# Kernel optimization log

Hardware: AMD Instinct MI355X
Metric: run time of the kernel (lower is better)

The kernel has to match this reference:

```python
import jax, jax.numpy as jnp
import numpy as np
from jax import lax

# Config (matches init_kwargs)
B, CIN, H, W = 32, 256, 56, 56
COUT, KS, STRIDE, PAD, GROUPS = 256, 3, 1, 1, 2
CG_IN = CIN // GROUPS            # 128
OUT_F = COUT // GROUPS           # 128 per-group out features
IN_F = CG_IN * KS * KS           # 1152 per-group in features
Q = (IN_F * OUT_F // 4) * GROUPS # 73728 quadruplets total
TAU = 1.0

# All six 2-of-4 masking patterns (as in the torch module)
_MASK_PATTERNS = np.array([[0.,0.,1.,1.],[0.,1.,0.,1.],[0.,1.,1.,0.],
                           [1.,0.,0.,1.],[1.,0.,1.,0.],[1.,1.,0.,0.]], dtype=np.float32)


def setup_inputs() -> dict:
    key = jax.random.key(0)
    k1, k2, k3, k4 = jax.random.split(key, 4)
    x = jax.random.normal(k1, (B, CIN, H, W), dtype=jnp.float32)
    # per-group weight blocks, xavier-ish scale
    Ws = jax.random.normal(k2, (GROUPS, OUT_F, IN_F), dtype=jnp.float32) * 0.03
    choice_weights = jax.random.normal(k3, (Q, 6), dtype=jnp.float32)
    # gumbel noise: -log(Exp(1)) ~ Gumbel(0,1), matching -empty.exponential_().log()
    gumbels = -jnp.log(jax.random.exponential(k4, (Q, 6), dtype=jnp.float32))
    masking_patterns = jnp.asarray(_MASK_PATTERNS)
    return {"x": x, "Ws": Ws, "choice_weights": choice_weights,
            "gumbels": gumbels, "masking_patterns": masking_patterns}


def _hard_gumbel_softmax(logits, gumbels, tau):
    # straight-through hard gumbel softmax over last dim
    y_soft = jax.nn.softmax((logits + gumbels) / tau, axis=-1)
    idx = jnp.argmax(y_soft, axis=-1)
    y_hard = jax.nn.one_hot(idx, logits.shape[-1], dtype=logits.dtype)
    return y_hard - lax.stop_gradient(y_soft) + y_soft


def reference(x, Ws, choice_weights, gumbels, masking_patterns):
    # 1) sample 2:4 mask per quadruplet via hard gumbel-softmax choice over 6 patterns
    choice = _hard_gumbel_softmax(choice_weights, gumbels, TAU)   # (Q, 6)
    mask = choice @ masking_patterns                              # (Q, 4)
    mask = mask.reshape(GROUPS, OUT_F, IN_F)                      # quadruplets tile W row-major
    Wm = Ws * mask                                                # (G, OUT_F, IN_F)

    # 2) im2col (torch Unfold ordering: channel-major, then kh, kw)
    patches = lax.conv_general_dilated_patches(
        x, filter_shape=(KS, KS), window_strides=(STRIDE, STRIDE),
        padding=[(PAD, PAD), (PAD, PAD)])                         # (B, CIN*KS*KS, Ho, Wo)
    Ho = (H + 2 * PAD - KS) // STRIDE + 1
    Wo = (W + 2 * PAD - KS) // STRIDE + 1
    L = Ho * Wo
    # channel-major ordering => group g occupies contiguous IN_F rows
    patches = patches.reshape(B, GROUPS, IN_F, L)                 # (B, G, IN_F, L)

    # 3) per-group masked GEMM, no bias (use_bias=False)
    y = jnp.einsum('goi,bgil->bgol', Wm, patches)                 # (B, G, OUT_F, L)
    return y.reshape(B, COUT, Ho, Wo)
```

## Files before the change

kernel.cpp:

```cpp
#include <hip/hip_runtime.h>


#define INF   1152
#define HO    56
#define LOUT  3136
#define XP    58
#define Q     73728

typedef __attribute__((ext_vector_type(8))) short bf16x8;
typedef __attribute__((ext_vector_type(4))) float f32x4;

__device__ __forceinline__ unsigned short f2bf(float f) {
  union { float f; unsigned u; } v; v.f = f;
  unsigned r = v.u + 0x7fffu + ((v.u >> 16) & 1u);
  return (unsigned short)(r >> 16);
}

__device__ __forceinline__ void async_load16(const void* g, void* l) {
  __builtin_amdgcn_global_load_lds(
      (const __attribute__((address_space(1))) void*)g,
      (__attribute__((address_space(3))) void*)l, 16, 0, 0);
}

__global__ __launch_bounds__(256) void gumbel_kernel(
    const float* __restrict__ cw, const float* __restrict__ gb,
    unsigned char* __restrict__ pmask) {
  int q = blockIdx.x * 256 + threadIdx.x;
  const float* cq = cw + q * 6;
  const float* gq = gb + q * 6;
  float best = cq[0] + gq[0]; int bi = 0;
  #pragma unroll
  for (int j = 1; j < 6; ++j) {
    float v = cq[j] + gq[j];
    if (v > best) { best = v; bi = j; }
  }
  pmask[q] = (unsigned char)bi;
}

__global__ __launch_bounds__(256) void pack_kernel(
    const float* __restrict__ Ws, const unsigned char* __restrict__ pmask,
    const float* __restrict__ pat, unsigned short* __restrict__ Wt) {
  int idx = blockIdx.x * 256 + threadIdx.x;
  int c   = idx & 127;
  int of  = (idx >> 7) & 127;
  int gt  = idx >> 14;
  int g   = gt / 9;
  int tap = gt - g * 9;
  int e   = ((g << 7) + of) * INF + c * 9 + tap;
  float m = pat[pmask[e >> 2] * 4 + (e & 3)];
  Wt[idx] = f2bf(Ws[e] * m);
}

__global__ __launch_bounds__(256) void xpose_kernel(const float* __restrict__ x,
                                                    unsigned short* __restrict__ Xt) {
  __shared__ float lds[56 * 129];
  const int t   = threadIdx.x;
  const int ihp = blockIdx.x;
  const int bg  = blockIdx.y;
  uint4* dst = (uint4*)(Xt + ((bg * XP + ihp) * XP) * 128);
  if (ihp == 0 || ihp == XP - 1) {
    const uint4 z = {0u, 0u, 0u, 0u};
    for (int i = t; i < XP * 16; i += 256) dst[i] = z;
    return;
  }
  const int ih = ihp - 1;
  const float4* src = (const float4*)(x + (bg * 128) * LOUT + ih * HO);
  for (int i = t; i < 128 * 14; i += 256) {
    int c = i / 14, seg = i - c * 14;
    float4 v = src[c * (LOUT / 4) + seg];
    float* row = &lds[(seg * 4) * 129 + c];
    row[0]       = v.x;
    row[129]     = v.y;
    row[2 * 129] = v.z;
    row[3 * 129] = v.w;
  }
  __syncthreads();
  for (int i = t; i < XP * 16; i += 256) {
    int iwp = i >> 4, oct = i & 15;
    uint4 val = {0u, 0u, 0u, 0u};
    if (iwp != 0 && iwp != XP - 1) {
      const float* s = &lds[(iwp - 1) * 129 + (oct << 3)];
      unsigned d0 = (unsigned)f2bf(s[0]) | ((unsigned)f2bf(s[1]) << 16);
      unsigned d1 = (unsigned)f2bf(s[2]) | ((unsigned)f2bf(s[3]) << 16);
      unsigned d2 = (unsigned)f2bf(s[4]) | ((unsigned)f2bf(s[5]) << 16);
      unsigned d3 = (unsigned)f2bf(s[6]) | ((unsigned)f2bf(s[7]) << 16);
      val.x = d0; val.y = d1; val.z = d2; val.w = d3;
    }
    dst[i] = val;
  }
}

__global__ __launch_bounds__(256, 4) void conv_mfma_kernel(
    const unsigned short* __restrict__ Wt, const unsigned short* __restrict__ Xt,
    float* __restrict__ out) {
  __shared__ __align__(16) unsigned short sA[128 * 32];
  __shared__ __align__(16) unsigned short sB[128 * 32];
  const int t  = threadIdx.x;
  const int ln = t & 63, wv = t >> 6;
  const int wm = wv >> 1, wn = wv & 1;
  const int col = ln & 15, kq = ln >> 4;

  const int lid   = blockIdx.y * 25 + blockIdx.x;
  const int v     = (lid & 7) * 200 + (lid >> 3);
  const int bg    = v / 25;
  const int tileN = v - bg * 25;
  const int g     = bg & 1;
  const int l0    = tileN << 7;

  const int kqs  = (t & 3) ^ ((t >> 3) & 3);
  const int c8   = kqs << 3;
  const int aoff = ((t >> 2) << 7) + c8;
  int boff[2];
  #pragma unroll
  for (int p = 0; p < 2; ++p) {
    int ll = l0 + (p << 6) + (t >> 2);
    if (ll > LOUT - 1) ll = LOUT - 1;
    int oh = ll / HO, ow = ll - oh * HO;
    boff[p] = ((bg * XP + oh) * XP + ow) * 128 + c8;
  }
  const int ldsw = (wv << 9);
  const int swk  = (kq ^ ((col >> 1) & 3)) << 3;

  f32x4 acc[4][4];
  #pragma unroll
  for (int i = 0; i < 4; ++i)
    #pragma unroll
    for (int j = 0; j < 4; ++j) acc[i][j] = (f32x4){0.f, 0.f, 0.f, 0.f};

  for (int tap = 0; tap < 9; ++tap) {
    const int th = tap / 3, tw = tap - th * 3;
    const int bTap = (th * XP + tw) << 7;
    const int aTap = (g * 9 + tap) << 14;
    #pragma unroll 1
    for (int kc = 0; kc < 4; ++kc) {
      const int c0 = kc << 5;
      __syncthreads();
      #pragma unroll
      for (int p = 0; p < 2; ++p) {
        async_load16(Wt + aTap + (p << 13) + aoff + c0, &sA[(p << 11) + ldsw]);
        async_load16(Xt + boff[p] + bTap + c0,          &sB[(p << 11) + ldsw]);
      }
      __syncthreads();
      bf16x8 af[4], bfr[4];
      #pragma unroll
      for (int mi = 0; mi < 4; ++mi)
        af[mi] = *(const bf16x8*)&sA[(wm << 11) + (((mi << 4) + col) << 5) + swk];
      #pragma unroll
      for (int ni = 0; ni < 4; ++ni)
        bfr[ni] = *(const bf16x8*)&sB[(wn << 11) + (((ni << 4) + col) << 5) + swk];
      #pragma unroll
      for (int mi = 0; mi < 4; ++mi)
        #pragma unroll
        for (int ni = 0; ni < 4; ++ni)
          acc[mi][ni] = __builtin_amdgcn_mfma_f32_16x16x32_bf16(
              af[mi], bfr[ni], acc[mi][ni], 0, 0, 0);
    }
  }

  const int rowq = kq << 2;
  #pragma unroll
  for (int mi = 0; mi < 4; ++mi) {
    #pragma unroll
    for (int ni = 0; ni < 4; ++ni) {
      const int l = l0 + (wn << 6) + (ni << 4) + col;
      if (l < LOUT) {
        #pragma unroll
        for (int r = 0; r < 4; ++r) {
          const int of = (wm << 6) + (mi << 4) + rowq + r;
          out[(bg * 128 + of) * LOUT + l] = acc[mi][ni][r];
        }
      }
    }
  }
}

extern "C" void kernel_launch(void* const* d_in, const int* in_sizes, int n_in,
                              void* d_out, int out_size, void* d_ws, size_t ws_size,
                              hipStream_t stream) {
  const float* x   = (const float*)d_in[0];
  const float* Ws  = (const float*)d_in[1];
  const float* cw  = (const float*)d_in[2];
  const float* gb  = (const float*)d_in[3];
  const float* pat = (const float*)d_in[4];
  float* out = (float*)d_out;

  unsigned short* Wt    = (unsigned short*)d_ws;
  unsigned char*  pmask = (unsigned char*)((char*)d_ws + 640 * 1024);
  unsigned short* Xt    = (unsigned short*)((char*)d_ws + (1 << 20));

  gumbel_kernel<<<Q / 256, 256, 0, stream>>>(cw, gb, pmask);
  xpose_kernel<<<dim3(XP, 64), 256, 0, stream>>>(x, Xt);
  pack_kernel<<<1152, 256, 0, stream>>>(Ws, pmask, pat, Wt);
  conv_mfma_kernel<<<dim3(25, 64), 256, 0, stream>>>(Wt, Xt, out);
}
```

Measured before the change: 278.0 us.

## Fuse prep kernels into one launch and double conv K-chunk to 64

Merges the gumbel argmax, weight pack and input transpose kernels into a single prep kernel whose blocks split by index. Each weight element recomputes the argmax over its quadruplet's six logits, which is redundant but removes the pmask round trip and two launches. The conv kernel now stages 64 channels per LDS chunk instead of 32, with a new XOR swizzle. This halves the sync barriers per tap and doubles LDS use per block, which may reduce occupancy.

```diff
diff --git a/kernel.cpp b/kernel.cpp
--- a/kernel.cpp
+++ b/kernel.cpp
@@ -5,7 +5,6 @@
 #define HO    56
 #define LOUT  3136
 #define XP    58
-#define Q     73728
 
 typedef __attribute__((ext_vector_type(8))) short bf16x8;
 typedef __attribute__((ext_vector_type(4))) float f32x4;
@@ -22,41 +21,38 @@
       (__attribute__((address_space(3))) void*)l, 16, 0, 0);
 }
 
-__global__ __launch_bounds__(256) void gumbel_kernel(
+__global__ __launch_bounds__(256) void prep_kernel(
+    const float* __restrict__ x, const float* __restrict__ Ws,
     const float* __restrict__ cw, const float* __restrict__ gb,
-    unsigned char* __restrict__ pmask) {
-  int q = blockIdx.x * 256 + threadIdx.x;
-  const float* cq = cw + q * 6;
-  const float* gq = gb + q * 6;
-  float best = cq[0] + gq[0]; int bi = 0;
-  #pragma unroll
-  for (int j = 1; j < 6; ++j) {
-    float v = cq[j] + gq[j];
-    if (v > best) { best = v; bi = j; }
-  }
-  pmask[q] = (unsigned char)bi;
-}
-
-__global__ __launch_bounds__(256) void pack_kernel(
-    const float* __restrict__ Ws, const unsigned char* __restrict__ pmask,
-    const float* __restrict__ pat, unsigned short* __restrict__ Wt) {
-  int idx = blockIdx.x * 256 + threadIdx.x;
-  int c   = idx & 127;
-  int of  = (idx >> 7) & 127;
-  int gt  = idx >> 14;
-  int g   = gt / 9;
-  int tap = gt - g * 9;
-  int e   = ((g << 7) + of) * INF + c * 9 + tap;
-  float m = pat[pmask[e >> 2] * 4 + (e & 3)];
-  Wt[idx] = f2bf(Ws[e] * m);
-}
-
-__global__ __launch_bounds__(256) void xpose_kernel(const float* __restrict__ x,
-                                                    unsigned short* __restrict__ Xt) {
+    const float* __restrict__ pat,
+    unsigned short* __restrict__ Xt, unsigned short* __restrict__ Wt) {
   __shared__ float lds[56 * 129];
   const int t   = threadIdx.x;
-  const int ihp = blockIdx.x;
-  const int bg  = blockIdx.y;
+  const int bid = blockIdx.x;
+
+  if (bid >= 3712) {
+    int idx = (bid - 3712) * 256 + t;
+    int c   = idx & 127;
+    int of  = (idx >> 7) & 127;
+    int gt  = idx >> 14;
+    int g   = gt / 9;
+    int tap = gt - g * 9;
+    int e   = ((g << 7) + of) * INF + c * 9 + tap;
+    int q   = e >> 2, pos = e & 3;
+    const float* cq = cw + q * 6;
+    const float* gq = gb + q * 6;
+    float best = cq[0] + gq[0]; int bi = 0;
+    #pragma unroll
+    for (int j = 1; j < 6; ++j) {
+      float v2 = cq[j] + gq[j];
+      if (v2 > best) { best = v2; bi = j; }
+    }
+    Wt[idx] = f2bf(Ws[e] * pat[bi * 4 + pos]);
+    return;
+  }
+
+  const int bg  = bid / 58;
+  const int ihp = bid - bg * 58;
   uint4* dst = (uint4*)(Xt + ((bg * XP + ihp) * XP) * 128);
   if (ihp == 0 || ihp == XP - 1) {
     const uint4 z = {0u, 0u, 0u, 0u};
@@ -80,11 +76,10 @@
     uint4 val = {0u, 0u, 0u, 0u};
     if (iwp != 0 && iwp != XP - 1) {
       const float* s = &lds[(iwp - 1) * 129 + (oct << 3)];
-      unsigned d0 = (unsigned)f2bf(s[0]) | ((unsigned)f2bf(s[1]) << 16);
-      unsigned d1 = (unsigned)f2bf(s[2]) | ((unsigned)f2bf(s[3]) << 16);
-      unsigned d2 = (unsigned)f2bf(s[4]) | ((unsigned)f2bf(s[5]) << 16);
-      unsigned d3 = (unsigned)f2bf(s[6]) | ((unsigned)f2bf(s[7]) << 16);
-      val.x = d0; val.y = d1; val.z = d2; val.w = d3;
+      val.x = (unsigned)f2bf(s[0]) | ((unsigned)f2bf(s[1]) << 16);
+      val.y = (unsigned)f2bf(s[2]) | ((unsigned)f2bf(s[3]) << 16);
+      val.z = (unsigned)f2bf(s[4]) | ((unsigned)f2bf(s[5]) << 16);
+      val.w = (unsigned)f2bf(s[6]) | ((unsigned)f2bf(s[7]) << 16);
     }
     dst[i] = val;
   }
@@ -93,12 +88,12 @@
 __global__ __launch_bounds__(256, 4) void conv_mfma_kernel(
     const unsigned short* __restrict__ Wt, const unsigned short* __restrict__ Xt,
     float* __restrict__ out) {
-  __shared__ __align__(16) unsigned short sA[128 * 32];
-  __shared__ __align__(16) unsigned short sB[128 * 32];
+  __shared__ __align__(16) unsigned short sA[128 * 64];
+  __shared__ __align__(16) unsigned short sB[128 * 64];
   const int t  = threadIdx.x;
   const int ln = t & 63, wv = t >> 6;
   const int wm = wv >> 1, wn = wv & 1;
-  const int col = ln & 15, kq = ln >> 4;
+  const int col = ln & 15, kq = ln >> 4, c7 = col & 7;
 
   const int lid   = blockIdx.y * 25 + blockIdx.x;
   const int v     = (lid & 7) * 200 + (lid >> 3);
@@ -107,19 +102,18 @@
   const int g     = bg & 1;
   const int l0    = tileN << 7;
 
-  const int kqs  = (t & 3) ^ ((t >> 3) & 3);
-  const int c8   = kqs << 3;
-  const int aoff = ((t >> 2) << 7) + c8;
-  int boff[2];
+  const int r8 = ln >> 3;
+  const int ch = (ln & 7) ^ r8;
+  int arow[4], brow[4];
   #pragma unroll
-  for (int p = 0; p < 2; ++p) {
-    int ll = l0 + (p << 6) + (t >> 2);
+  for (int i = 0; i < 4; ++i) {
+    const int rr = (wv << 5) + (i << 3) + r8;
+    arow[i] = (rr << 7) + (ch << 3);
+    int ll = l0 + rr;
     if (ll > LOUT - 1) ll = LOUT - 1;
     int oh = ll / HO, ow = ll - oh * HO;
-    boff[p] = ((bg * XP + oh) * XP + ow) * 128 + c8;
+    brow[i] = ((bg * XP + oh) * XP + ow) * 128 + (ch << 3);
   }
-  const int ldsw = (wv << 9);
-  const int swk  = (kq ^ ((col >> 1) & 3)) << 3;
 
   f32x4 acc[4][4];
   #pragma unroll
@@ -132,28 +126,33 @@
     const int bTap = (th * XP + tw) << 7;
     const int aTap = (g * 9 + tap) << 14;
     #pragma unroll 1
-    for (int kc = 0; kc < 4; ++kc) {
-      const int c0 = kc << 5;
+    for (int kc = 0; kc < 2; ++kc) {
+      const int c0 = kc << 6;
       __syncthreads();
       #pragma unroll
-      for (int p = 0; p < 2; ++p) {
-        async_load16(Wt + aTap + (p << 13) + aoff + c0, &sA[(p << 11) + ldsw]);
-        async_load16(Xt + boff[p] + bTap + c0,          &sB[(p << 11) + ldsw]);
+      for (int i = 0; i < 4; ++i) {
+        const int lb = ((wv << 5) + (i << 3)) << 6;
+        async_load16(Wt + aTap + c0 + arow[i], &sA[lb]);
+        async_load16(Xt + bTap + c0 + brow[i], &sB[lb]);
       }
       __syncthreads();
-      bf16x8 af[4], bfr[4];
       #pragma unroll
-      for (int mi = 0; mi < 4; ++mi)
-        af[mi] = *(const bf16x8*)&sA[(wm << 11) + (((mi << 4) + col) << 5) + swk];
-      #pragma unroll
-      for (int ni = 0; ni < 4; ++ni)
-        bfr[ni] = *(const bf16x8*)&sB[(wn << 11) + (((ni << 4) + col) << 5) + swk];
-      #pragma unroll
-      for (int mi = 0; mi < 4; ++mi)
+      for (int kh = 0; kh < 2; ++kh) {
+        const int pk = (((kh << 2) + kq) ^ c7) << 3;
+        bf16x8 af[4], bfr[4];
+        #pragma unroll
+        for (int mi = 0; mi < 4; ++mi)
+          af[mi] = *(const bf16x8*)&sA[(((wm << 6) + (mi << 4) + col) << 6) + pk];
         #pragma unroll
         for (int ni = 0; ni < 4; ++ni)
-          acc[mi][ni] = __builtin_amdgcn_mfma_f32_16x16x32_bf16(
-              af[mi], bfr[ni], acc[mi][ni], 0, 0, 0);
+          bfr[ni] = *(const bf16x8*)&sB[(((wn << 6) + (ni << 4) + col) << 6) + pk];
+        #pragma unroll
+        for (int mi = 0; mi < 4; ++mi)
+          #pragma unroll
+          for (int ni = 0; ni < 4; ++ni)
+            acc[mi][ni] = __builtin_amdgcn_mfma_f32_16x16x32_bf16(
+                af[mi], bfr[ni], acc[mi][ni], 0, 0, 0);
+      }
     }
   }
 
@@ -184,12 +183,9 @@
   const float* pat = (const float*)d_in[4];
   float* out = (float*)d_out;
 
-  unsigned short* Wt    = (unsigned short*)d_ws;
-  unsigned char*  pmask = (unsigned char*)((char*)d_ws + 640 * 1024);
-  unsigned short* Xt    = (unsigned short*)((char*)d_ws + (1 << 20));
+  unsigned short* Wt = (unsigned short*)d_ws;
+  unsigned short* Xt = (unsigned short*)((char*)d_ws + (1 << 20));
 
-  gumbel_kernel<<<Q / 256, 256, 0, stream>>>(cw, gb, pmask);
-  xpose_kernel<<<dim3(XP, 64), 256, 0, stream>>>(x, Xt);
-  pack_kernel<<<1152, 256, 0, stream>>>(Ws, pmask, pat, Wt);
+  prep_kernel<<<4864, 256, 0, stream>>>(x, Ws, cw, gb, pat, Xt, Wt);
   conv_mfma_kernel<<<dim3(25, 64), 256, 0, stream>>>(Wt, Xt, out);
 }
```

Measured after the change: 253.6 us. 8.8% less time.
